# Kernel optimization log

Hardware: AMD Instinct MI355X
Metric: run time of the kernel (lower is better)

## Reference

```python
import jax, jax.numpy as jnp
import numpy as np

N = 50000
E = 800000
D_IN = 128
D_OUT = 128


def setup_inputs() -> dict:
    key = jax.random.key(0)
    ks = jax.random.split(key, 12)
    x = jax.random.normal(ks[0], (N, D_IN), dtype=jnp.float32)
    W1 = jax.random.normal(ks[1], (D_IN, D_OUT), dtype=jnp.float32) * (1.0 / np.sqrt(D_IN))
    b1 = jnp.zeros((D_OUT,), dtype=jnp.float32)
    W2 = jax.random.normal(ks[2], (D_IN, D_OUT), dtype=jnp.float32) * (1.0 / np.sqrt(D_IN))
    b2 = jnp.zeros((D_OUT,), dtype=jnp.float32)
    # inverted-dropout masks, p=0.5 -> values in {0, 2}
    def mask(k):
        return jnp.where(jax.random.uniform(k, (N, D_IN)) < 0.5, 0.0, 2.0).astype(jnp.float32)
    mask_pos1 = mask(ks[3])
    mask_neg1 = mask(ks[4])
    mask_pos2 = mask(ks[5])
    mask_neg2 = mask(ks[6])
    edge_index1 = jax.random.randint(ks[7], (2, E), 0, N, dtype=jnp.int32)
    edge_index2 = jax.random.randint(ks[8], (2, E), 0, N, dtype=jnp.int32)
    perm1 = jax.random.permutation(ks[9], N).astype(jnp.int32)
    perm2 = jax.random.permutation(ks[10], N).astype(jnp.int32)
    return dict(x=x, W1=W1, b1=b1, W2=W2, b2=b2,
                mask_pos1=mask_pos1, mask_neg1=mask_neg1,
                mask_pos2=mask_pos2, mask_neg2=mask_neg2,
                edge_index1=edge_index1, edge_index2=edge_index2,
                perm1=perm1, perm2=perm2)


def gcn_conv(x, W, b, edge_index):
    """PyG GCNConv: add self-loops, symmetric normalization, then x@W aggregation + bias."""
    n = x.shape[0]
    xw = x @ W  # [N, D_OUT]
    loops = jnp.arange(n, dtype=edge_index.dtype)
    src = jnp.concatenate([edge_index[0], loops])
    dst = jnp.concatenate([edge_index[1], loops])
    deg = jax.ops.segment_sum(jnp.ones_like(dst, dtype=xw.dtype), dst, num_segments=n)
    dinv = jax.lax.rsqrt(jnp.maximum(deg, 1.0))  # deg >= 1 due to self-loops
    norm = dinv[src] * dinv[dst]                 # [E+N]
    msg = xw[src] * norm[:, None]                # [E+N, D_OUT]
    out = jax.ops.segment_sum(msg, dst, num_segments=n)
    return out + b


def _branch(x, W, b, edge_index, mask_pos, mask_neg, perm):
    pos_h = jax.nn.relu(gcn_conv(x * mask_pos, W, b, edge_index))
    neg_in = (x * mask_neg)[perm]
    neg_h = jax.nn.relu(gcn_conv(neg_in, W, b, edge_index))
    summary = jnp.mean(pos_h, axis=0, keepdims=True)  # [1, D_OUT]
    return pos_h, neg_h, summary


def reference(x, W1, b1, W2, b2, mask_pos1, mask_neg1, mask_pos2, mask_neg2,
              edge_index1, edge_index2, perm1, perm2):
    p1, n1, s1 = _branch(x, W1, b1, edge_index1, mask_pos1, mask_neg1, perm1)
    p2, n2, s2 = _branch(x, W2, b2, edge_index2, mask_pos2, mask_neg2, perm2)
    return (p1, n1, s1, p2, n2, s2)
```

## Files before the change

### kernel.cpp

```cpp
#include <hip/hip_runtime.h>
#include <hip/hip_fp16.h>

#define NN 50000
#define NE 800000
#define D 128
#define BKT_BLOCKS 1024
#define GEMM_JOBS 3128
#define GEMMB 1043
#define NBKT 64
#define BW 782
#define SCAP 2048

typedef _Float16 half8_t __attribute__((ext_vector_type(8)));
typedef _Float16 half4_t __attribute__((ext_vector_type(4)));
typedef float f32x4 __attribute__((ext_vector_type(4)));

__global__ void k_init(float* s1, float* s2, int* bcnt,
                       const float* __restrict__ W1, const float* __restrict__ W2,
                       _Float16* wt1, _Float16* wt2,
                       const int* __restrict__ perm1, const int* __restrict__ perm2,
                       int* pinv1, int* pinv2) {
    int i = blockIdx.x * 256 + threadIdx.x;
    if (i < NN) { pinv1[perm1[i]] = i; pinv2[perm2[i]] = i; }
    if (i < 1024) bcnt[i] = 0;
    if (i < D) { s1[i] = 0.f; s2[i] = 0.f; }
    if (i < 16384) {
        int n = i >> 7, k = i & 127;
        wt1[n * 128 + k] = (_Float16)W1[k * 128 + n];
        wt2[n * 128 + k] = (_Float16)W2[k * 128 + n];
    }
}

__launch_bounds__(256)
__global__ void k_bucket_gemm(const int* __restrict__ src1, const int* __restrict__ dst1,
                              const int* __restrict__ src2, const int* __restrict__ dst2,
                              int* bcnt, int2* bsd1, int2* bsd2,
                              const _Float16* __restrict__ wt1, const _Float16* __restrict__ wt2,
                              const float* __restrict__ x,
                              const float* __restrict__ mp1, const float* __restrict__ mn1,
                              const float* __restrict__ mp2, const float* __restrict__ mn2,
                              const int* __restrict__ pinv1, const int* __restrict__ pinv2,
                              _Float16* xwi1, _Float16* xwi2) {
    __shared__ __align__(16) union SU {
        struct { int lcnt[128], lpos[128], gbase[128]; } b;
        _Float16 st[4][16][136];
    } U;
    int t = threadIdx.x;
    int bid = blockIdx.x;

    if (bid < BKT_BLOCKS) {
        int sl = bid & 7;
        if (t < 128) { U.b.lcnt[t] = 0; U.b.lpos[t] = 0; }
        __syncthreads();

        int e0 = bid * 256 + t;
        int s1v0=0,d1v0=0,s2v0=0,d2v0=0, s1v1=0,d1v1=0,s2v1=0,d2v1=0;
        int s1v2=0,d1v2=0,s2v2=0,d2v2=0, s1v3=0,d1v3=0,s2v3=0,d2v3=0;
        bool v0 = (e0 + 0 * 262144) < NE;
        bool v1 = (e0 + 1 * 262144) < NE;
        bool v2 = (e0 + 2 * 262144) < NE;
        bool v3 = (e0 + 3 * 262144) < NE;
        if (v0) { int e = e0;             s1v0 = src1[e]; d1v0 = dst1[e]; s2v0 = src2[e]; d2v0 = dst2[e]; }
        if (v1) { int e = e0 + 262144;    s1v1 = src1[e]; d1v1 = dst1[e]; s2v1 = src2[e]; d2v1 = dst2[e]; }
        if (v2) { int e = e0 + 2*262144;  s1v2 = src1[e]; d1v2 = dst1[e]; s2v2 = src2[e]; d2v2 = dst2[e]; }
        if (v3) { int e = e0 + 3*262144;  s1v3 = src1[e]; d1v3 = dst1[e]; s2v3 = src2[e]; d2v3 = dst2[e]; }

        if (v0) { atomicAdd(&U.b.lcnt[d1v0 / BW], 1); atomicAdd(&U.b.lcnt[NBKT + d2v0 / BW], 1); }
        if (v1) { atomicAdd(&U.b.lcnt[d1v1 / BW], 1); atomicAdd(&U.b.lcnt[NBKT + d2v1 / BW], 1); }
        if (v2) { atomicAdd(&U.b.lcnt[d1v2 / BW], 1); atomicAdd(&U.b.lcnt[NBKT + d2v2 / BW], 1); }
        if (v3) { atomicAdd(&U.b.lcnt[d1v3 / BW], 1); atomicAdd(&U.b.lcnt[NBKT + d2v3 / BW], 1); }
        __syncthreads();
        if (t < 128) U.b.gbase[t] = atomicAdd(&bcnt[t * 8 + sl], U.b.lcnt[t]);
        __syncthreads();

        #define PLACE(sv, dv) { \
            int r = (dv) / BW; \
            int p = U.b.gbase[r] + atomicAdd(&U.b.lpos[r], 1); \
            if (p < SCAP) bsd1[(r * 8 + sl) * SCAP + p] = make_int2((sv), (dv)); }
        #define PLACE2(sv, dv) { \
            int r = (dv) / BW; \
            int p = U.b.gbase[NBKT + r] + atomicAdd(&U.b.lpos[NBKT + r], 1); \
            if (p < SCAP) bsd2[(r * 8 + sl) * SCAP + p] = make_int2((sv), (dv)); }
        if (v0) { PLACE(s1v0, d1v0); PLACE2(s2v0, d2v0); }
        if (v1) { PLACE(s1v1, d1v1); PLACE2(s2v1, d2v1); }
        if (v2) { PLACE(s1v2, d1v2); PLACE2(s2v2, d2v2); }
        if (v3) { PLACE(s1v3, d1v3); PLACE2(s2v3, d2v3); }
        #undef PLACE
        #undef PLACE2
        return;
    }

    int gb = bid - BKT_BLOCKS;
    int wave = t >> 6;
    int lane = t & 63;
    int quad = lane >> 4;
    int m = lane & 15;

    #pragma unroll 1
    for (int k = 0; k < 3; k++) {
        int j = gb + k * GEMMB;
        if (j >= GEMM_JOBS) break;
        int which = j / 782;
        int bx = j - which * 782;
        int tile = bx * 4 + wave;
        if (tile * 16 >= NN) continue;

        const _Float16* wt = (which < 2) ? wt1 : wt2;
        const float* mask = (which == 0) ? mp1 : (which == 1) ? mn1 : (which == 2) ? mp2 : mn2;
        const int* pinv = (which == 1) ? pinv1 : (which == 3) ? pinv2 : nullptr;
        _Float16* out = ((which < 2) ? xwi1 : xwi2) + ((which & 1) ? 128 : 0);

        int row = tile * 16 + m;
        const float* xrow = x + (long)row * D;
        const float* mrow = mask + (long)row * D;

        half8_t a[4];
        #pragma unroll
        for (int kk = 0; kk < 4; kk++) {
            int k0 = kk * 32 + quad * 8;
            f32x4 xa = *(const f32x4*)(xrow + k0);
            f32x4 xb = *(const f32x4*)(xrow + k0 + 4);
            f32x4 ma = __builtin_nontemporal_load((const f32x4*)(mrow + k0));
            f32x4 mb = __builtin_nontemporal_load((const f32x4*)(mrow + k0 + 4));
            a[kk][0] = (_Float16)(xa[0] * ma[0]);
            a[kk][1] = (_Float16)(xa[1] * ma[1]);
            a[kk][2] = (_Float16)(xa[2] * ma[2]);
            a[kk][3] = (_Float16)(xa[3] * ma[3]);
            a[kk][4] = (_Float16)(xb[0] * mb[0]);
            a[kk][5] = (_Float16)(xb[1] * mb[1]);
            a[kk][6] = (_Float16)(xb[2] * mb[2]);
            a[kk][7] = (_Float16)(xb[3] * mb[3]);
        }

        f32x4 accs[8];
        #pragma unroll
        for (int nt = 0; nt < 8; nt++) {
            const _Float16* wrow = wt + (nt * 16 + m) * 128 + quad * 8;
            f32x4 acc = {0.f, 0.f, 0.f, 0.f};
            #pragma unroll
            for (int kk = 0; kk < 4; kk++) {
                half8_t w = *(const half8_t*)(wrow + kk * 32);
                acc = __builtin_amdgcn_mfma_f32_16x16x32_f16(w, a[kk], acc, 0, 0, 0);
            }
            accs[nt] = acc;
        }

        int orow = pinv ? pinv[row] : row;
        _Float16* st = &U.st[wave][0][0];

        #pragma unroll
        for (int nt = 0; nt < 8; nt++) {
            half4_t h;
            h[0] = (_Float16)accs[nt][0];
            h[1] = (_Float16)accs[nt][1];
            h[2] = (_Float16)accs[nt][2];
            h[3] = (_Float16)accs[nt][3];
            *(half4_t*)(st + m * 136 + nt * 16 + quad * 4) = h;
        }
        #pragma unroll
        for (int p = 0; p < 4; p++) {
            int cc = (lane >> 4) + p * 4;
            half8_t v = *(const half8_t*)(st + m * 136 + cc * 8);
            *(half8_t*)(out + (long)orow * 256 + cc * 8) = v;
        }
    }
}

__launch_bounds__(512)
__global__ void k_build(const int* __restrict__ bcnt,
                        const int2* __restrict__ bsd1, const int2* __restrict__ bsd2,
                        int* rp1, int* rp2, int* col1, int* col2,
                        float* dinv1, float* dinv2) {
    __shared__ int h[1024];
    __shared__ int tsum[512];
    __shared__ int tb[64];
    __shared__ int ns[8];
    __shared__ int bbase;
    int t = threadIdx.x;
    int g = blockIdx.x >> 6;
    int f = blockIdx.x & 63;
    const int2* bsd = (g ? bsd2 : bsd1) + f * 8 * SCAP;
    int* rp = g ? rp2 : rp1;
    int* col = g ? col2 : col1;
    float* dinv = g ? dinv2 : dinv1;

    h[t] = 0; h[t + 512] = 0;
    if (t < 8) {
        int v = bcnt[(g * NBKT + f) * 8 + t];
        ns[t] = (v > SCAP) ? SCAP : v;
    }
    if (t < NBKT) {
        int tot = 0;
        #pragma unroll
        for (int s = 0; s < 8; s++) tot += bcnt[(g * NBKT + t) * 8 + s];
        tb[t] = tot;
    }
    __syncthreads();

    #pragma unroll
    for (int s = 0; s < 8; s++) {
        int n = ns[s];
        const int2* seg = bsd + s * SCAP;
        for (int i = t; i < n; i += 512) atomicAdd(&h[seg[i].y - f * BW], 1);
    }
    __syncthreads();
    if (t == 0) { int b = 0; for (int j = 0; j < f; j++) b += tb[j]; bbase = b; }

    int a0 = h[2 * t], a1 = h[2 * t + 1];
    int s = a0 + a1;
    tsum[t] = s;
    __syncthreads();
    for (int off = 1; off < 512; off <<= 1) {
        int add = (t >= off) ? tsum[t - off] : 0;
        __syncthreads();
        tsum[t] += add;
        __syncthreads();
    }
    int excl = tsum[t] - s + bbase;
    int idx = 2 * t, gd = f * BW + idx;
    int e0 = excl, e1 = excl + a0;
    h[2 * t] = e0; h[2 * t + 1] = e1;
    if (idx < BW && gd < NN)         { rp[gd]     = e0; dinv[gd]     = rsqrtf((float)(a0 + 1)); }
    if (idx + 1 < BW && gd + 1 < NN) { rp[gd + 1] = e1; dinv[gd + 1] = rsqrtf((float)(a1 + 1)); }
    if (f == 63 && t == 0) rp[NN] = NE;
    __syncthreads();

    #pragma unroll
    for (int sg = 0; sg < 8; sg++) {
        int n = ns[sg];
        const int2* seg = bsd + sg * SCAP;
        for (int i = t; i < n; i += 512) {
            int2 e = seg[i];
            int p = atomicAdd(&h[e.y - f * BW], 1);
            col[p] = e.x;
        }
    }
}

__launch_bounds__(256)
__global__ void k_agg(const _Float16* __restrict__ xwi1, const _Float16* __restrict__ xwi2,
                      const int* __restrict__ rp1, const int* __restrict__ col1,
                      const float* __restrict__ dinv1,
                      const int* __restrict__ rp2, const int* __restrict__ col2,
                      const float* __restrict__ dinv2,
                      const float* __restrict__ b1, const float* __restrict__ b2,
                      float* out) {
    int g = blockIdx.y;
    const _Float16* xwi = g ? xwi2 : xwi1;
    const int* rp = g ? rp2 : rp1;
    const int* col = g ? col2 : col1;
    const float* dinv = g ? dinv2 : dinv1;
    const float* bias = g ? b2 : b1;
    float* pos_out = out + (g ? 12800128L : 0L);
    float* neg_out = out + (g ? 19200128L : 6400000L);

    int t = threadIdx.x;
    int wave = t >> 6, lane = t & 63;
    int i = blockIdx.x * 4 + wave;
    if (i >= NN) return;
    int j4 = lane * 4;

    float di = dinv[i];
    half4_t sv = *(const half4_t*)(xwi + (long)i * 256 + j4);
    float a0 = di * (float)sv[0], a1 = di * (float)sv[1];
    float a2 = di * (float)sv[2], a3 = di * (float)sv[3];
    int e0 = rp[i], e1 = rp[i + 1];
    int e = e0;
    for (; e + 8 <= e1; e += 8) {
        int s0 = col[e + 0], s1 = col[e + 1], s2 = col[e + 2], s3 = col[e + 3];
        int s4 = col[e + 4], s5 = col[e + 5], s6 = col[e + 6], s7 = col[e + 7];
        float ds0 = dinv[s0], ds1 = dinv[s1], ds2 = dinv[s2], ds3 = dinv[s3];
        float ds4 = dinv[s4], ds5 = dinv[s5], ds6 = dinv[s6], ds7 = dinv[s7];
        half4_t v0 = *(const half4_t*)(xwi + (long)s0 * 256 + j4);
        half4_t v1 = *(const half4_t*)(xwi + (long)s1 * 256 + j4);
        half4_t v2 = *(const half4_t*)(xwi + (long)s2 * 256 + j4);
        half4_t v3 = *(const half4_t*)(xwi + (long)s3 * 256 + j4);
        half4_t v4 = *(const half4_t*)(xwi + (long)s4 * 256 + j4);
        half4_t v5 = *(const half4_t*)(xwi + (long)s5 * 256 + j4);
        half4_t v6 = *(const half4_t*)(xwi + (long)s6 * 256 + j4);
        half4_t v7 = *(const half4_t*)(xwi + (long)s7 * 256 + j4);
        a0 += ds0*(float)v0[0] + ds1*(float)v1[0] + ds2*(float)v2[0] + ds3*(float)v3[0]
            + ds4*(float)v4[0] + ds5*(float)v5[0] + ds6*(float)v6[0] + ds7*(float)v7[0];
        a1 += ds0*(float)v0[1] + ds1*(float)v1[1] + ds2*(float)v2[1] + ds3*(float)v3[1]
            + ds4*(float)v4[1] + ds5*(float)v5[1] + ds6*(float)v6[1] + ds7*(float)v7[1];
        a2 += ds0*(float)v0[2] + ds1*(float)v1[2] + ds2*(float)v2[2] + ds3*(float)v3[2]
            + ds4*(float)v4[2] + ds5*(float)v5[2] + ds6*(float)v6[2] + ds7*(float)v7[2];
        a3 += ds0*(float)v0[3] + ds1*(float)v1[3] + ds2*(float)v2[3] + ds3*(float)v3[3]
            + ds4*(float)v4[3] + ds5*(float)v5[3] + ds6*(float)v6[3] + ds7*(float)v7[3];
    }
    for (; e + 4 <= e1; e += 4) {
        int s0 = col[e + 0], s1 = col[e + 1], s2 = col[e + 2], s3 = col[e + 3];
        float ds0 = dinv[s0], ds1 = dinv[s1], ds2 = dinv[s2], ds3 = dinv[s3];
        half4_t v0 = *(const half4_t*)(xwi + (long)s0 * 256 + j4);
        half4_t v1 = *(const half4_t*)(xwi + (long)s1 * 256 + j4);
        half4_t v2 = *(const half4_t*)(xwi + (long)s2 * 256 + j4);
        half4_t v3 = *(const half4_t*)(xwi + (long)s3 * 256 + j4);
        a0 += ds0*(float)v0[0] + ds1*(float)v1[0] + ds2*(float)v2[0] + ds3*(float)v3[0];
        a1 += ds0*(float)v0[1] + ds1*(float)v1[1] + ds2*(float)v2[1] + ds3*(float)v3[1];
        a2 += ds0*(float)v0[2] + ds1*(float)v1[2] + ds2*(float)v2[2] + ds3*(float)v3[2];
        a3 += ds0*(float)v0[3] + ds1*(float)v1[3] + ds2*(float)v2[3] + ds3*(float)v3[3];
    }
    for (; e < e1; e++) {
        int s = col[e];
        float ds = dinv[s];
        half4_t v = *(const half4_t*)(xwi + (long)s * 256 + j4);
        a0 += ds*(float)v[0]; a1 += ds*(float)v[1]; a2 += ds*(float)v[2]; a3 += ds*(float)v[3];
    }
    int jj = (lane < 32) ? j4 : (j4 - 128);
    const f32x4* bp = (const f32x4*)(bias + jj);
    f32x4 bv = *bp;
    f32x4 o;
    o[0] = fmaxf(0.f, di * a0 + bv[0]);
    o[1] = fmaxf(0.f, di * a1 + bv[1]);
    o[2] = fmaxf(0.f, di * a2 + bv[2]);
    o[3] = fmaxf(0.f, di * a3 + bv[3]);
    float* dst = ((lane < 32) ? pos_out : neg_out) + (long)i * D + jj;
    __builtin_nontemporal_store(o, (f32x4*)dst);
}

__launch_bounds__(256)
__global__ void k_sum(const float* __restrict__ pos1, const float* __restrict__ pos2,
                      float* s1, float* s2) {
    int g = blockIdx.y;
    const float* pos = g ? pos2 : pos1;
    float* s = g ? s2 : s1;
    int t = threadIdx.x;
    int rg = t >> 5;
    int j = (t & 31) * 4;
    f32x4 acc = {0.f, 0.f, 0.f, 0.f};
    for (int i = blockIdx.x * 8 + rg; i < NN; i += gridDim.x * 8) {
        f32x4 v = __builtin_nontemporal_load((const f32x4*)(pos + (long)i * D + j));
        acc[0] += v[0]; acc[1] += v[1]; acc[2] += v[2]; acc[3] += v[3];
    }
    __shared__ float sm[8][128];
    sm[rg][j + 0] = acc[0];
    sm[rg][j + 1] = acc[1];
    sm[rg][j + 2] = acc[2];
    sm[rg][j + 3] = acc[3];
    __syncthreads();
    if (t < 128) {
        float v = 0.f;
        for (int r = 0; r < 8; r++) v += sm[r][t];
        atomicAdd(&s[t], v * (1.0f / NN));
    }
}

extern "C" void kernel_launch(void* const* d_in, const int* in_sizes, int n_in,
                              void* d_out, int out_size, void* d_ws, size_t ws_size,
                              hipStream_t stream) {
    const float* x   = (const float*)d_in[0];
    const float* W1  = (const float*)d_in[1];
    const float* b1  = (const float*)d_in[2];
    const float* W2  = (const float*)d_in[3];
    const float* b2  = (const float*)d_in[4];
    const float* mp1 = (const float*)d_in[5];
    const float* mn1 = (const float*)d_in[6];
    const float* mp2 = (const float*)d_in[7];
    const float* mn2 = (const float*)d_in[8];
    const int* e1 = (const int*)d_in[9];
    const int* e2 = (const int*)d_in[10];
    const int* perm1 = (const int*)d_in[11];
    const int* perm2 = (const int*)d_in[12];
    const int* src1 = e1;       const int* dst1 = e1 + NE;
    const int* src2 = e2;       const int* dst2 = e2 + NE;
    float* out = (float*)d_out;

    char* w = (char*)d_ws;
    _Float16* xwi1 = (_Float16*)w; w += (size_t)NN * 256 * 2;
    _Float16* xwi2 = (_Float16*)w; w += (size_t)NN * 256 * 2;
    int* rp1 = (int*)w;   w += (size_t)(NN + 4) * 4;
    int* rp2 = (int*)w;   w += (size_t)(NN + 4) * 4;
    int* col1 = (int*)w;  w += (size_t)NE * 4;
    int* col2 = (int*)w;  w += (size_t)NE * 4;
    float* dinv1 = (float*)w; w += (size_t)NN * 4;
    float* dinv2 = (float*)w; w += (size_t)NN * 4;
    int* bcnt  = (int*)w; w += (size_t)1024 * 4;
    int2* bsd1 = (int2*)w; w += (size_t)NBKT * 8 * SCAP * 8;
    int2* bsd2 = (int2*)w; w += (size_t)NBKT * 8 * SCAP * 8;
    _Float16* wt1 = (_Float16*)w; w += (size_t)D * D * 2;
    _Float16* wt2 = (_Float16*)w; w += (size_t)D * D * 2;
    int* pinv1 = (int*)w; w += (size_t)NN * 4;
    int* pinv2 = (int*)w; w += (size_t)NN * 4;

    float* s1 = out + 12800000L;
    float* s2 = out + 25600128L;
    const float* pos1 = out;
    const float* pos2 = out + 12800128L;

    k_init<<<dim3(196), 256, 0, stream>>>(s1, s2, bcnt, W1, W2, wt1, wt2,
                                          perm1, perm2, pinv1, pinv2);
    k_bucket_gemm<<<dim3(BKT_BLOCKS + GEMMB), 256, 0, stream>>>(
        src1, dst1, src2, dst2, bcnt, bsd1, bsd2,
        wt1, wt2, x, mp1, mn1, mp2, mn2, pinv1, pinv2, xwi1, xwi2);
    k_build<<<dim3(128), 512, 0, stream>>>(bcnt, bsd1, bsd2,
                                           rp1, rp2, col1, col2, dinv1, dinv2);
    k_agg<<<dim3(12500, 2), 256, 0, stream>>>(xwi1, xwi2,
                                              rp1, col1, dinv1, rp2, col2, dinv2,
                                              b1, b2, out);
    k_sum<<<dim3(512, 2), 256, 0, stream>>>(pos1, pos2, s1, s2);
}
```

Baseline: 468.1 us.

## Sort CSR columns by source octant and give each GEMM job its own block

```diff
diff --git a/kernel.cpp b/kernel.cpp
--- a/kernel.cpp
+++ b/kernel.cpp
@@ -5,10 +5,10 @@
 #define NE 800000
 #define D 128
 #define BKT_BLOCKS 1024
-#define GEMM_JOBS 3128
-#define GEMMB 1043
+#define GEMM_BLOCKS 3128
 #define NBKT 64
 #define BW 782
+#define OCT 6250
 #define SCAP 2048
 
 typedef _Float16 half8_t __attribute__((ext_vector_type(8)));
@@ -90,79 +90,73 @@
         return;
     }
 
-    int gb = bid - BKT_BLOCKS;
+    int g = bid - BKT_BLOCKS;
+    int which = g / 782;
+    int bx = g - which * 782;
+    const _Float16* wt = (which < 2) ? wt1 : wt2;
+    const float* mask = (which == 0) ? mp1 : (which == 1) ? mn1 : (which == 2) ? mp2 : mn2;
+    const int* pinv = (which == 1) ? pinv1 : (which == 3) ? pinv2 : nullptr;
+    _Float16* out = ((which < 2) ? xwi1 : xwi2) + ((which & 1) ? 128 : 0);
+
     int wave = t >> 6;
     int lane = t & 63;
     int quad = lane >> 4;
     int m = lane & 15;
-
-    #pragma unroll 1
-    for (int k = 0; k < 3; k++) {
-        int j = gb + k * GEMMB;
-        if (j >= GEMM_JOBS) break;
-        int which = j / 782;
-        int bx = j - which * 782;
-        int tile = bx * 4 + wave;
-        if (tile * 16 >= NN) continue;
-
-        const _Float16* wt = (which < 2) ? wt1 : wt2;
-        const float* mask = (which == 0) ? mp1 : (which == 1) ? mn1 : (which == 2) ? mp2 : mn2;
-        const int* pinv = (which == 1) ? pinv1 : (which == 3) ? pinv2 : nullptr;
-        _Float16* out = ((which < 2) ? xwi1 : xwi2) + ((which & 1) ? 128 : 0);
-
-        int row = tile * 16 + m;
-        const float* xrow = x + (long)row * D;
-        const float* mrow = mask + (long)row * D;
-
-        half8_t a[4];
+    int tile = bx * 4 + wave;
+    if (tile * 16 >= NN) return;
+
+    int row = tile * 16 + m;
+    const float* xrow = x + (long)row * D;
+    const float* mrow = mask + (long)row * D;
+
+    half8_t a[4];
+    #pragma unroll
+    for (int kk = 0; kk < 4; kk++) {
+        int k0 = kk * 32 + quad * 8;
+        f32x4 xa = *(const f32x4*)(xrow + k0);
+        f32x4 xb = *(const f32x4*)(xrow + k0 + 4);
+        f32x4 ma = __builtin_nontemporal_load((const f32x4*)(mrow + k0));
+        f32x4 mb = __builtin_nontemporal_load((const f32x4*)(mrow + k0 + 4));
+        a[kk][0] = (_Float16)(xa[0] * ma[0]);
+        a[kk][1] = (_Float16)(xa[1] * ma[1]);
+        a[kk][2] = (_Float16)(xa[2] * ma[2]);
+        a[kk][3] = (_Float16)(xa[3] * ma[3]);
+        a[kk][4] = (_Float16)(xb[0] * mb[0]);
+        a[kk][5] = (_Float16)(xb[1] * mb[1]);
+        a[kk][6] = (_Float16)(xb[2] * mb[2]);
+        a[kk][7] = (_Float16)(xb[3] * mb[3]);
+    }
+
+    f32x4 accs[8];
+    #pragma unroll
+    for (int nt = 0; nt < 8; nt++) {
+        const _Float16* wrow = wt + (nt * 16 + m) * 128 + quad * 8;
+        f32x4 acc = {0.f, 0.f, 0.f, 0.f};
         #pragma unroll
         for (int kk = 0; kk < 4; kk++) {
-            int k0 = kk * 32 + quad * 8;
-            f32x4 xa = *(const f32x4*)(xrow + k0);
-            f32x4 xb = *(const f32x4*)(xrow + k0 + 4);
-            f32x4 ma = __builtin_nontemporal_load((const f32x4*)(mrow + k0));
-            f32x4 mb = __builtin_nontemporal_load((const f32x4*)(mrow + k0 + 4));
-            a[kk][0] = (_Float16)(xa[0] * ma[0]);
-            a[kk][1] = (_Float16)(xa[1] * ma[1]);
-            a[kk][2] = (_Float16)(xa[2] * ma[2]);
-            a[kk][3] = (_Float16)(xa[3] * ma[3]);
-            a[kk][4] = (_Float16)(xb[0] * mb[0]);
-            a[kk][5] = (_Float16)(xb[1] * mb[1]);
-            a[kk][6] = (_Float16)(xb[2] * mb[2]);
-            a[kk][7] = (_Float16)(xb[3] * mb[3]);
+            half8_t w = *(const half8_t*)(wrow + kk * 32);
+            acc = __builtin_amdgcn_mfma_f32_16x16x32_f16(w, a[kk], acc, 0, 0, 0);
         }
-
-        f32x4 accs[8];
-        #pragma unroll
-        for (int nt = 0; nt < 8; nt++) {
-            const _Float16* wrow = wt + (nt * 16 + m) * 128 + quad * 8;
-            f32x4 acc = {0.f, 0.f, 0.f, 0.f};
-            #pragma unroll
-            for (int kk = 0; kk < 4; kk++) {
-                half8_t w = *(const half8_t*)(wrow + kk * 32);
-                acc = __builtin_amdgcn_mfma_f32_16x16x32_f16(w, a[kk], acc, 0, 0, 0);
-            }
-            accs[nt] = acc;
-        }
-
-        int orow = pinv ? pinv[row] : row;
-        _Float16* st = &U.st[wave][0][0];
-
-        #pragma unroll
-        for (int nt = 0; nt < 8; nt++) {
-            half4_t h;
-            h[0] = (_Float16)accs[nt][0];
-            h[1] = (_Float16)accs[nt][1];
-            h[2] = (_Float16)accs[nt][2];
-            h[3] = (_Float16)accs[nt][3];
-            *(half4_t*)(st + m * 136 + nt * 16 + quad * 4) = h;
-        }
-        #pragma unroll
-        for (int p = 0; p < 4; p++) {
-            int cc = (lane >> 4) + p * 4;
-            half8_t v = *(const half8_t*)(st + m * 136 + cc * 8);
-            *(half8_t*)(out + (long)orow * 256 + cc * 8) = v;
-        }
+        accs[nt] = acc;
+    }
+
+    int orow = pinv ? pinv[row] : row;
+    _Float16* st = &U.st[wave][0][0];
+
+    #pragma unroll
+    for (int nt = 0; nt < 8; nt++) {
+        half4_t h;
+        h[0] = (_Float16)accs[nt][0];
+        h[1] = (_Float16)accs[nt][1];
+        h[2] = (_Float16)accs[nt][2];
+        h[3] = (_Float16)accs[nt][3];
+        *(half4_t*)(st + m * 136 + nt * 16 + quad * 4) = h;
+    }
+    #pragma unroll
+    for (int p = 0; p < 4; p++) {
+        int cc = (lane >> 4) + p * 4;
+        half8_t v = *(const half8_t*)(st + m * 136 + cc * 8);
+        *(half8_t*)(out + (long)orow * 256 + cc * 8) = v;
     }
 }
 
@@ -171,7 +165,7 @@
                         const int2* __restrict__ bsd1, const int2* __restrict__ bsd2,
                         int* rp1, int* rp2, int* col1, int* col2,
                         float* dinv1, float* dinv2) {
-    __shared__ int h[1024];
+    __shared__ int h2[6272];
     __shared__ int tsum[512];
     __shared__ int tb[64];
     __shared__ int ns[8];
@@ -184,30 +178,36 @@
     int* col = g ? col2 : col1;
     float* dinv = g ? dinv2 : dinv1;
 
-    h[t] = 0; h[t + 512] = 0;
+    for (int q = t; q < 6272; q += 512) h2[q] = 0;
     if (t < 8) {
         int v = bcnt[(g * NBKT + f) * 8 + t];
         ns[t] = (v > SCAP) ? SCAP : v;
     }
     if (t < NBKT) {
         int tot = 0;
-        #pragma unroll
         for (int s = 0; s < 8; s++) tot += bcnt[(g * NBKT + t) * 8 + s];
         tb[t] = tot;
     }
     __syncthreads();
 
-    #pragma unroll
     for (int s = 0; s < 8; s++) {
         int n = ns[s];
         const int2* seg = bsd + s * SCAP;
-        for (int i = t; i < n; i += 512) atomicAdd(&h[seg[i].y - f * BW], 1);
+        for (int i = t; i < n; i += 512)
+            atomicAdd(&h2[(seg[i].y - f * BW) * 8 + seg[i].x / OCT], 1);
     }
     __syncthreads();
     if (t == 0) { int b = 0; for (int j = 0; j < f; j++) b += tb[j]; bbase = b; }
 
-    int a0 = h[2 * t], a1 = h[2 * t + 1];
-    int s = a0 + a1;
+    int d0 = 2 * t, d1 = 2 * t + 1;
+    int cnt0 = 0, cnt1 = 0;
+    if (d0 < BW) {
+        for (int o = 0; o < 8; o++) cnt0 += h2[d0 * 8 + o];
+    }
+    if (d1 < BW) {
+        for (int o = 0; o < 8; o++) cnt1 += h2[d1 * 8 + o];
+    }
+    int s = cnt0 + cnt1;
     tsum[t] = s;
     __syncthreads();
     for (int off = 1; off < 512; off <<= 1) {
@@ -217,21 +217,28 @@
         __syncthreads();
     }
     int excl = tsum[t] - s + bbase;
-    int idx = 2 * t, gd = f * BW + idx;
-    int e0 = excl, e1 = excl + a0;
-    h[2 * t] = e0; h[2 * t + 1] = e1;
-    if (idx < BW && gd < NN)         { rp[gd]     = e0; dinv[gd]     = rsqrtf((float)(a0 + 1)); }
-    if (idx + 1 < BW && gd + 1 < NN) { rp[gd + 1] = e1; dinv[gd + 1] = rsqrtf((float)(a1 + 1)); }
+    int base0 = excl, base1 = excl + cnt0;
+    int gd = f * BW + d0;
+    if (d0 < BW && gd < NN)     { rp[gd]     = base0; dinv[gd]     = rsqrtf((float)(cnt0 + 1)); }
+    if (d1 < BW && gd + 1 < NN) { rp[gd + 1] = base1; dinv[gd + 1] = rsqrtf((float)(cnt1 + 1)); }
     if (f == 63 && t == 0) rp[NN] = NE;
+
+    if (d0 < BW) {
+        int run = base0;
+        for (int o = 0; o < 8; o++) { int c = h2[d0 * 8 + o]; h2[d0 * 8 + o] = run; run += c; }
+    }
+    if (d1 < BW) {
+        int run = base1;
+        for (int o = 0; o < 8; o++) { int c = h2[d1 * 8 + o]; h2[d1 * 8 + o] = run; run += c; }
+    }
     __syncthreads();
 
-    #pragma unroll
     for (int sg = 0; sg < 8; sg++) {
         int n = ns[sg];
         const int2* seg = bsd + sg * SCAP;
         for (int i = t; i < n; i += 512) {
             int2 e = seg[i];
-            int p = atomicAdd(&h[e.y - f * BW], 1);
+            int p = atomicAdd(&h2[(e.y - f * BW) * 8 + e.x / OCT], 1);
             col[p] = e.x;
         }
     }
@@ -389,7 +396,7 @@
 
     k_init<<<dim3(196), 256, 0, stream>>>(s1, s2, bcnt, W1, W2, wt1, wt2,
                                           perm1, perm2, pinv1, pinv2);
-    k_bucket_gemm<<<dim3(BKT_BLOCKS + GEMMB), 256, 0, stream>>>(
+    k_bucket_gemm<<<dim3(BKT_BLOCKS + GEMM_BLOCKS), 256, 0, stream>>>(
         src1, dst1, src2, dst2, bcnt, bsd1, bsd2,
         wt1, wt2, x, mp1, mn1, mp2, mn2, pinv1, pinv2, xwi1, xwi2);
     k_build<<<dim3(128), 512, 0, stream>>>(bcnt, bsd1, bsd2,
```

After: 458.6 us. 1.02x faster.
